# Performance work log

Hardware: AMD Instinct MI355X
Metric: run time of the kernel (lower is better)

Reference implementation:

```python
import jax, jax.numpy as jnp
import numpy as np

N = 100000
E = 3200000
IN_DIM = 512
HID = 256
NUM_CLASSES = 16
P_DROP = 0.5
EPS_BN = 1e-5


def setup_inputs() -> dict:
    key = jax.random.key(0)
    ks = jax.random.split(key, 6)
    x = jax.random.normal(ks[0], (N, IN_DIM), jnp.float32)
    edge_src = jax.random.randint(ks[1], (E,), 0, N, dtype=jnp.int32)
    edge_dst = jax.random.randint(ks[2], (E,), 0, N, dtype=jnp.int32)
    # Glorot-ish init for GraphConv weights (bias=False in the module)
    W1 = jax.random.normal(ks[3], (IN_DIM, HID), jnp.float32) / np.sqrt(IN_DIM).astype(np.float32)
    W2 = jax.random.normal(ks[4], (HID, NUM_CLASSES), jnp.float32) / np.sqrt(HID).astype(np.float32)
    W3 = jax.random.normal(ks[5], (HID, NUM_CLASSES), jnp.float32) / np.sqrt(HID).astype(np.float32)
    return {"x": x, "W1": W1, "W2": W2, "W3": W3,
            "edge_src": edge_src, "edge_dst": edge_dst}


def _graph_conv(h, W, edge_src, edge_dst, out_inv_sqrt, in_inv_sqrt):
    # DGL GraphConv, norm='both', bias=False:
    #   rst = D_in^{-1/2} * A_agg( D_out^{-1/2} * h @ W )
    # Apply W before aggregation (out_dim <= in_dim here); same math as DGL.
    h = h * out_inv_sqrt[:, None]          # [N, d_in]
    h = h @ W                              # [N, d_out]
    agg = jax.ops.segment_sum(h[edge_src], edge_dst, num_segments=h.shape[0])
    return agg * in_inv_sqrt[:, None]


def _dropout(key, x, p=P_DROP):
    keep = jax.random.bernoulli(key, 1.0 - p, x.shape)
    return jnp.where(keep, x / (1.0 - p), jnp.zeros((), x.dtype))


def reference(x, W1, W2, W3, edge_src, edge_dst):
    n = x.shape[0]
    ones = jnp.ones(edge_src.shape[0], x.dtype)
    out_deg = jax.ops.segment_sum(ones, edge_src, num_segments=n)
    in_deg = jax.ops.segment_sum(ones, edge_dst, num_segments=n)
    out_is = jnp.maximum(out_deg, 1.0) ** -0.5   # DGL clamps degree to min 1
    in_is = jnp.maximum(in_deg, 1.0) ** -0.5

    k1, k2a, k2b, keps = jax.random.split(jax.random.key(42), 4)

    # gc1 + relu
    h = _dropout(k1, x)
    h = jax.nn.relu(_graph_conv(h, W1, edge_src, edge_dst, out_is, in_is))

    # BatchNorm1d(affine=False, track_running_stats=False): batch stats
    mean = jnp.mean(h, axis=0)
    var = jnp.var(h, axis=0)
    h = (h - mean) * jax.lax.rsqrt(var + EPS_BN)

    # gc2 (mu) and gc3 (logvar), each with its own dropout of hidden1
    mu = _graph_conv(_dropout(k2a, h), W2, edge_src, edge_dst, out_is, in_is)
    logvar = _graph_conv(_dropout(k2b, h), W3, edge_src, edge_dst, out_is, in_is)

    # reparameterize (training): eps * exp(logvar) + mu  (note: exp(logvar), per source)
    eps = jax.random.normal(keps, mu.shape, mu.dtype)
    return eps * jnp.exp(logvar) + mu
```

## Files before the change

kernel.cpp:

```cpp
#include <hip/hip_runtime.h>
#include <stdint.h>

#define N_NODES 100000
#define N_EDGES 3200000
#define IN_DIM  512
#define HID     256
#define NCLS    16

#define DBLK   256
#define DCHUNK (N_EDGES / DBLK)
#define DWIN2  50000

typedef unsigned short u16;
typedef __attribute__((ext_vector_type(8))) short short8;
typedef __attribute__((ext_vector_type(4))) float float4v;

__device__ __forceinline__ float bf2f(u16 u) {
  return __uint_as_float(((uint32_t)u) << 16);
}
__device__ __forceinline__ u16 f2bf(float f) {
  uint32_t u = __float_as_uint(f);
  return (u16)((u + 0x7fffu + ((u >> 16) & 1u)) >> 16);
}
__device__ __forceinline__ void acc8(float* a, uint4 v) {
  a[0] += bf2f((u16)(v.x & 0xffffu)); a[1] += bf2f((u16)(v.x >> 16));
  a[2] += bf2f((u16)(v.y & 0xffffu)); a[3] += bf2f((u16)(v.y >> 16));
  a[4] += bf2f((u16)(v.z & 0xffffu)); a[5] += bf2f((u16)(v.z >> 16));
  a[6] += bf2f((u16)(v.w & 0xffffu)); a[7] += bf2f((u16)(v.w >> 16));
}

__device__ __forceinline__ void gload16(const void* g, void* l) {
  __builtin_amdgcn_global_load_lds(
      (const __attribute__((address_space(1))) uint32_t*)g,
      (__attribute__((address_space(3))) uint32_t*)l, 16, 0, 0);
}

__host__ __device__ __forceinline__ uint32_t rotl32(uint32_t v, int d) {
  return (v << d) | (v >> (32 - d));
}

__host__ __device__ __forceinline__ void threefry2x32(uint32_t k0, uint32_t k1,
    uint32_t x0, uint32_t x1, uint32_t& o0, uint32_t& o1) {
  uint32_t ks0 = k0, ks1 = k1, ks2 = k0 ^ k1 ^ 0x1BD11BDAu;
  x0 += ks0; x1 += ks1;
#define TF_R(r) { x0 += x1; x1 = rotl32(x1, r); x1 ^= x0; }
  TF_R(13) TF_R(15) TF_R(26) TF_R(6)
  x0 += ks1; x1 += ks2 + 1u;
  TF_R(17) TF_R(29) TF_R(16) TF_R(24)
  x0 += ks2; x1 += ks0 + 2u;
  TF_R(13) TF_R(15) TF_R(26) TF_R(6)
  x0 += ks0; x1 += ks1 + 3u;
  TF_R(17) TF_R(29) TF_R(16) TF_R(24)
  x0 += ks1; x1 += ks2 + 4u;
  TF_R(13) TF_R(15) TF_R(26) TF_R(6)
  x0 += ks2; x1 += ks0 + 5u;
#undef TF_R
  o0 = x0; o1 = x1;
}

__host__ __device__ __forceinline__ uint32_t tf_bits32(uint32_t k0, uint32_t k1, uint32_t idx) {
  uint32_t o0, o1;
  threefry2x32(k0, k1, 0u, idx, o0, o1);
  return o0 ^ o1;
}

__device__ __forceinline__ float erfinv_f32(float x) {
  float w = -log1pf(-x * x);
  float p;
  if (w < 5.0f) {
    w -= 2.5f;
    p = 2.81022636e-08f;
    p = fmaf(p, w, 3.43273939e-07f);
    p = fmaf(p, w, -3.5233877e-06f);
    p = fmaf(p, w, -4.39150654e-06f);
    p = fmaf(p, w, 0.00021858087f);
    p = fmaf(p, w, -0.00125372503f);
    p = fmaf(p, w, -0.00417768164f);
    p = fmaf(p, w, 0.246640727f);
    p = fmaf(p, w, 1.50140941f);
  } else {
    w = sqrtf(w) - 3.0f;
    p = -0.000200214257f;
    p = fmaf(p, w, 0.000100950558f);
    p = fmaf(p, w, 0.00134934322f);
    p = fmaf(p, w, -0.00367342844f);
    p = fmaf(p, w, 0.00573950773f);
    p = fmaf(p, w, -0.0076224613f);
    p = fmaf(p, w, 0.00943887047f);
    p = fmaf(p, w, 1.00167406f);
    p = fmaf(p, w, 2.83297682f);
  }
  return p * x;
}

__global__ __launch_bounds__(1024) void hist_k(
    const int* __restrict__ esrc, const int* __restrict__ edst,
    u16* __restrict__ P16) {
  __shared__ uint32_t h32[DWIN2 / 2];
  const int b = blockIdx.x, tid = threadIdx.x;
  const int ebase = b * DCHUNK;
  for (int w = 0; w < 2; ++w) {
    const int lo = w * DWIN2;
    for (int i = tid; i < DWIN2 / 2; i += 1024) h32[i] = 0u;
    __syncthreads();
    for (int e = ebase + tid; e < ebase + DCHUNK; e += 1024) {
      int s = esrc[e], d = edst[e];
      unsigned su = (unsigned)(s - lo);
      if (su < (unsigned)DWIN2) atomicAdd(&h32[su >> 1], 1u << ((su & 1) * 16));
      unsigned du = (unsigned)(d - lo);
      if (du < (unsigned)DWIN2) atomicAdd(&h32[du >> 1], 0x100u << ((du & 1) * 16));
    }
    __syncthreads();
    for (int i = tid; i < DWIN2 / 2; i += 1024) {
      *(uint32_t*)(P16 + (size_t)b * N_NODES + lo + 2 * i) = h32[i];
    }
    __syncthreads();
  }
}

__global__ void degsum_k(u16* __restrict__ P16, int* __restrict__ ind,
                         float* __restrict__ out_is, float* __restrict__ in_is) {
  int n = blockIdx.x * 256 + threadIdx.x;
  if (n >= N_NODES) return;
  uint32_t to = 0, ti = 0;
#pragma unroll 8
  for (int b = 0; b < DBLK; ++b) {
    uint32_t v = P16[(size_t)b * N_NODES + n];
    P16[(size_t)b * N_NODES + n] = (u16)ti;
    to += v & 0xffu; ti += v >> 8;
  }
  ind[n] = (int)ti;
  out_is[n] = rsqrtf(fmaxf((float)to, 1.0f));
  in_is[n]  = rsqrtf(fmaxf((float)ti, 1.0f));
}

__global__ __launch_bounds__(1024) void scan_offsets_k(
    const int* __restrict__ ind, int* __restrict__ row_ofs) {
  __shared__ int wsum[16];
  const int tid = threadIdx.x;
  const int lane = tid & 63, wv = tid >> 6;
  int running = 0;
  for (int base = 0; base < N_NODES; base += 1024) {
    const int i = base + tid;
    int v = (i < N_NODES) ? ind[i] : 0;
    int sc = v;
#pragma unroll
    for (int d = 1; d < 64; d <<= 1) {
      int t = __shfl_up(sc, d, 64);
      if (lane >= d) sc += t;
    }
    if (lane == 63) wsum[wv] = sc;
    __syncthreads();
    if (wv == 0) {
      int t = (lane < 16) ? wsum[lane] : 0;
#pragma unroll
      for (int d = 1; d < 16; d <<= 1) {
        int u = __shfl_up(t, d, 64);
        if (lane >= d) t += u;
      }
      if (lane < 16) wsum[lane] = t;
    }
    __syncthreads();
    int wbase = (wv > 0) ? wsum[wv - 1] : 0;
    if (i < N_NODES) row_ofs[i] = running + wbase + sc - v;
    running += wsum[15];
    __syncthreads();
  }
  if (tid == 0) row_ofs[N_NODES] = running;
}

__global__ __launch_bounds__(1024) void place_k(
    const int* __restrict__ esrc, const int* __restrict__ edst,
    const u16* __restrict__ P16, const int* __restrict__ row_ofs,
    int* __restrict__ csr) {
  __shared__ uint32_t cur32[N_NODES / 4];
  const int b = blockIdx.x, tid = threadIdx.x;
  for (int i = tid; i < N_NODES / 4; i += 1024) cur32[i] = 0u;
  __syncthreads();
  const int ebase = b * DCHUNK;
  for (int e = ebase + tid; e < ebase + DCHUNK; e += 1024) {
    int d = edst[e];
    int base = row_ofs[d] + (int)P16[(size_t)b * N_NODES + d];
    uint32_t old = atomicAdd(&cur32[d >> 2], 1u << ((d & 3) * 8));
    int c = (int)((old >> ((d & 3) * 8)) & 0xffu);
    csr[base + c] = esrc[e];
  }
}

__global__ void cast_w_k(const float* __restrict__ W1, const float* __restrict__ W2,
                         const float* __restrict__ W3, u16* __restrict__ W1t,
                         u16* __restrict__ Wt23) {
  int idx = blockIdx.x * blockDim.x + threadIdx.x;
  if (idx < IN_DIM * HID) {
    int k = idx >> 8, n = idx & 255;
    W1t[n * IN_DIM + k] = f2bf(W1[idx]);
  } else {
    int t = idx - IN_DIM * HID;
    int n = t >> 8, k = t & 255;
    float v = (n < 16) ? W2[k * NCLS + n] : W3[k * NCLS + (n - 16)];
    Wt23[n * HID + k] = f2bf(v);
  }
}

#define G1_BM 128
#define G1_BKC 8
__global__ __launch_bounds__(512, 2) void gemm1_k(
    const float* __restrict__ x, const float* __restrict__ out_is,
    uint32_t k0, uint32_t k1,
    const u16* __restrict__ W1t, u16* __restrict__ X1b) {
  __shared__ u16 As[G1_BM * 64];
  __shared__ u16 Bs[256 * 64];
  const int tid = threadIdx.x;
  const int wid = tid >> 6, lane = tid & 63;
  const int wr = wid >> 2, wc = wid & 3;
  const int m16 = lane & 15, q = lane >> 4;
  const int srow = lane >> 3, schunk = lane & 7;
  const long base_row = (long)blockIdx.x * G1_BM;

  const int arow_l = tid >> 2, acp = tid & 3;
  const long agrow = base_row + arow_l;
  const long asrow = (agrow < N_NODES) ? agrow : (N_NODES - 1);
  const float asc = 2.0f * out_is[asrow];
  const float* xrow = x + asrow * IN_DIM;
  const int aw0 = ((2 * acp)     ^ (arow_l & 7)) * 8;
  const int aw1 = ((2 * acp + 1) ^ (arow_l & 7)) * 8;

  float4v acc[4][4];
#pragma unroll
  for (int i = 0; i < 4; ++i)
#pragma unroll
    for (int j = 0; j < 4; ++j) acc[i][j] = (float4v)0.0f;

  for (int ks = 0; ks < IN_DIM / 64; ++ks) {
    const int kbase = ks * 64 + acp * 16;
    float4 f0 = *(const float4*)(xrow + kbase);
    float4 f1 = *(const float4*)(xrow + kbase + 4);
    float4 f2 = *(const float4*)(xrow + kbase + 8);
    float4 f3 = *(const float4*)(xrow + kbase + 12);
    float xv[16] = {f0.x, f0.y, f0.z, f0.w, f1.x, f1.y, f1.z, f1.w,
                    f2.x, f2.y, f2.z, f2.w, f3.x, f3.y, f3.z, f3.w};
    const uint32_t ibase = (uint32_t)asrow * IN_DIM + (uint32_t)kbase;
    u16 ob[16];
#pragma unroll
    for (int j = 0; j < 16; ++j) {
      uint32_t bits = tf_bits32(k0, k1, ibase + (uint32_t)j);
      ob[j] = f2bf((bits >> 31) ? 0.0f : xv[j] * asc);
    }
    uint4 pka, pkb;
    pka.x = (uint32_t)ob[0] | ((uint32_t)ob[1] << 16);
    pka.y = (uint32_t)ob[2] | ((uint32_t)ob[3] << 16);
    pka.z = (uint32_t)ob[4] | ((uint32_t)ob[5] << 16);
    pka.w = (uint32_t)ob[6] | ((uint32_t)ob[7] << 16);
    pkb.x = (uint32_t)ob[8] | ((uint32_t)ob[9] << 16);
    pkb.y = (uint32_t)ob[10] | ((uint32_t)ob[11] << 16);
    pkb.z = (uint32_t)ob[12] | ((uint32_t)ob[13] << 16);
    pkb.w = (uint32_t)ob[14] | ((uint32_t)ob[15] << 16);
    *(uint4*)(As + arow_l * 64 + aw0) = pka;
    *(uint4*)(As + arow_l * 64 + aw1) = pkb;
#pragma unroll
    for (int i = 0; i < 4; ++i) {
      int j = wid * 4 + i;
      int n = j * 8 + srow;
      int gch = ks * G1_BKC + (schunk ^ (n & 7));
      gload16(W1t + (size_t)n * IN_DIM + gch * 8, Bs + j * 512);
    }
    __syncthreads();
#pragma unroll
    for (int kk = 0; kk < 2; ++kk) {
      short8 a[4], b[4];
      const int kq = kk * 4 + q;
      const int c = kq ^ (m16 & 7);
#pragma unroll
      for (int rt = 0; rt < 4; ++rt) {
        int row = wr * 64 + rt * 16 + m16;
        a[rt] = *(const short8*)(As + row * 64 + c * 8);
      }
#pragma unroll
      for (int ct = 0; ct < 4; ++ct) {
        int n = wc * 64 + ct * 16 + m16;
        b[ct] = *(const short8*)(Bs + n * 64 + c * 8);
      }
#pragma unroll
      for (int rt = 0; rt < 4; ++rt)
#pragma unroll
        for (int ct = 0; ct < 4; ++ct)
          acc[rt][ct] = __builtin_amdgcn_mfma_f32_16x16x32_bf16(a[rt], b[ct], acc[rt][ct], 0, 0, 0);
    }
    __syncthreads();
  }
#pragma unroll
  for (int rt = 0; rt < 4; ++rt) {
#pragma unroll
    for (int r = 0; r < 4; ++r) {
      long grow = base_row + wr * 64 + rt * 16 + q * 4 + r;
      if (grow < N_NODES) {
#pragma unroll
        for (int ct = 0; ct < 4; ++ct)
          X1b[grow * HID + wc * 64 + ct * 16 + m16] = f2bf(acc[rt][ct][r]);
      }
    }
  }
}

__global__ __launch_bounds__(256) void agg_relu_k(
    const u16* __restrict__ X1b, const int* __restrict__ row_ofs,
    const int* __restrict__ csr, const float* __restrict__ in_is,
    u16* __restrict__ h1b) {
  int d = blockIdx.x * 4 + (threadIdx.x >> 6);
  int lane = threadIdx.x & 63;
  int half = lane >> 5;
  int col = (lane & 31) * 8;
  int beg = row_ofs[d], end = row_ofs[d + 1];
  float a[8];
#pragma unroll
  for (int i = 0; i < 8; ++i) a[i] = 0.0f;
  int j = beg + half;
  for (; j + 14 < end; j += 16) {
    int s0 = csr[j],      s1 = csr[j + 2],  s2 = csr[j + 4],  s3 = csr[j + 6];
    int s4 = csr[j + 8],  s5 = csr[j + 10], s6 = csr[j + 12], s7 = csr[j + 14];
    uint4 v0 = *(const uint4*)(X1b + (size_t)s0 * HID + col);
    uint4 v1 = *(const uint4*)(X1b + (size_t)s1 * HID + col);
    uint4 v2 = *(const uint4*)(X1b + (size_t)s2 * HID + col);
    uint4 v3 = *(const uint4*)(X1b + (size_t)s3 * HID + col);
    uint4 v4 = *(const uint4*)(X1b + (size_t)s4 * HID + col);
    uint4 v5 = *(const uint4*)(X1b + (size_t)s5 * HID + col);
    uint4 v6 = *(const uint4*)(X1b + (size_t)s6 * HID + col);
    uint4 v7 = *(const uint4*)(X1b + (size_t)s7 * HID + col);
    acc8(a, v0); acc8(a, v1); acc8(a, v2); acc8(a, v3);
    acc8(a, v4); acc8(a, v5); acc8(a, v6); acc8(a, v7);
  }
  for (; j + 6 < end; j += 8) {
    int s0 = csr[j], s1 = csr[j + 2], s2 = csr[j + 4], s3 = csr[j + 6];
    uint4 v0 = *(const uint4*)(X1b + (size_t)s0 * HID + col);
    uint4 v1 = *(const uint4*)(X1b + (size_t)s1 * HID + col);
    uint4 v2 = *(const uint4*)(X1b + (size_t)s2 * HID + col);
    uint4 v3 = *(const uint4*)(X1b + (size_t)s3 * HID + col);
    acc8(a, v0); acc8(a, v1); acc8(a, v2); acc8(a, v3);
  }
  for (; j < end; j += 2) {
    uint4 v0 = *(const uint4*)(X1b + (size_t)csr[j] * HID + col);
    acc8(a, v0);
  }
#pragma unroll
  for (int i = 0; i < 8; ++i) a[i] += __shfl(a[i], lane ^ 32, 64);
  if (half == 0) {
    float is = in_is[d];
    u16 o[8];
#pragma unroll
    for (int i = 0; i < 8; ++i) o[i] = f2bf(fmaxf(a[i] * is, 0.0f));
    uint4 pk;
    pk.x = (uint32_t)o[0] | ((uint32_t)o[1] << 16);
    pk.y = (uint32_t)o[2] | ((uint32_t)o[3] << 16);
    pk.z = (uint32_t)o[4] | ((uint32_t)o[5] << 16);
    pk.w = (uint32_t)o[6] | ((uint32_t)o[7] << 16);
    *(uint4*)(h1b + (size_t)d * HID + col) = pk;
  }
}

__global__ __launch_bounds__(256) void bn_stats_k(const u16* __restrict__ h1b,
                                                  float* __restrict__ bn) {
  __shared__ float ls[512];
  const int tid = threadIdx.x;
  const int cb = (tid & 31) * 8;
  const int ms = tid >> 5;
  float s[8], s2[8];
#pragma unroll
  for (int i = 0; i < 8; ++i) { s[i] = 0.f; s2[i] = 0.f; }
  for (int m = ms;; m += 8) {
    int r = blockIdx.x + 256 * m;
    if (r >= N_NODES) break;
    uint4 v = *(const uint4*)(h1b + (size_t)r * HID + cb);
    float f[8];
    f[0] = bf2f((u16)(v.x & 0xffffu)); f[1] = bf2f((u16)(v.x >> 16));
    f[2] = bf2f((u16)(v.y & 0xffffu)); f[3] = bf2f((u16)(v.y >> 16));
    f[4] = bf2f((u16)(v.z & 0xffffu)); f[5] = bf2f((u16)(v.z >> 16));
    f[6] = bf2f((u16)(v.w & 0xffffu)); f[7] = bf2f((u16)(v.w >> 16));
#pragma unroll
    for (int i = 0; i < 8; ++i) { s[i] += f[i]; s2[i] += f[i] * f[i]; }
  }
  ls[tid] = 0.f; ls[tid + 256] = 0.f;
  __syncthreads();
#pragma unroll
  for (int i = 0; i < 8; ++i) {
    atomicAdd(&ls[cb + i], s[i]);
    atomicAdd(&ls[256 + cb + i], s2[i]);
  }
  __syncthreads();
  atomicAdd(&bn[tid], ls[tid]);
  atomicAdd(&bn[HID + tid], ls[256 + tid]);
}

#define WLS 264
__global__ __launch_bounds__(256) void gemm23_k(
    const u16* __restrict__ h1b, const u16* __restrict__ Wt23,
    uint32_t ka0, uint32_t ka1, uint32_t kb0, uint32_t kb1,
    const float* __restrict__ out_is, const float* __restrict__ bn,
    u16* __restrict__ XMLV) {
  __shared__ u16 Wls[32 * WLS];
  __shared__ float cB[HID], cA[HID];
  const int tid = threadIdx.x;
#pragma unroll
  for (int i = 0; i < 4; ++i) {
    int idx = tid + i * 256;
    int n = idx >> 5, c = idx & 31;
    *(uint4*)(Wls + n * WLS + c * 8) = ((const uint4*)Wt23)[idx];
  }
  {
    float mean = bn[tid] * (1.0f / (float)N_NODES);
    float var = bn[HID + tid] * (1.0f / (float)N_NODES) - mean * mean;
    float istd = rsqrtf(var + 1e-5f);
    cB[tid] = istd;
    cA[tid] = -mean * istd;
  }
  __syncthreads();

  const int wv = tid >> 6, lane = tid & 63;
  const int m = lane & 15, q = lane >> 4;
  const long arow = (long)blockIdx.x * 64 + wv * 16 + m;
  const bool valid = arow < N_NODES;
  const float osc = valid ? 2.0f * out_is[arow] : 0.0f;
  const uint32_t rbase = (uint32_t)(valid ? arow : 0) * HID;

  float4v accM = (float4v)0.0f, accL = (float4v)0.0f;
  for (int kc = 0; kc < HID; kc += 32) {
    const int kof = kc + q * 8;
    uint4 hv = make_uint4(0, 0, 0, 0);
    if (valid) hv = *(const uint4*)(h1b + arow * HID + kof);
    float4 B0 = *(const float4*)(cB + kof);
    float4 B1 = *(const float4*)(cB + kof + 4);
    float4 A0 = *(const float4*)(cA + kof);
    float4 A1 = *(const float4*)(cA + kof + 4);
    float hval[8] = {
      bf2f((u16)(hv.x & 0xffffu)), bf2f((u16)(hv.x >> 16)),
      bf2f((u16)(hv.y & 0xffffu)), bf2f((u16)(hv.y >> 16)),
      bf2f((u16)(hv.z & 0xffffu)), bf2f((u16)(hv.z >> 16)),
      bf2f((u16)(hv.w & 0xffffu)), bf2f((u16)(hv.w >> 16))};
    float nb[8] = {B0.x, B0.y, B0.z, B0.w, B1.x, B1.y, B1.z, B1.w};
    float na[8] = {A0.x, A0.y, A0.z, A0.w, A1.x, A1.y, A1.z, A1.w};
    const uint32_t ibase = rbase + (uint32_t)kof;
    short8 Aa, Ab;
#pragma unroll
    for (int jj = 0; jj < 8; ++jj) {
      float t = fmaf(hval[jj], nb[jj], na[jj]) * osc;
      u16 tb = f2bf(t);
      uint32_t ba = tf_bits32(ka0, ka1, ibase + (uint32_t)jj);
      uint32_t bb = tf_bits32(kb0, kb1, ibase + (uint32_t)jj);
      Aa[jj] = (short)((ba >> 31) ? 0 : tb);
      Ab[jj] = (short)((bb >> 31) ? 0 : tb);
    }
    short8 Bm = *(const short8*)(Wls + m * WLS + kof);
    short8 Bl = *(const short8*)(Wls + (16 + m) * WLS + kof);
    accM = __builtin_amdgcn_mfma_f32_16x16x32_bf16(Aa, Bm, accM, 0, 0, 0);
    accL = __builtin_amdgcn_mfma_f32_16x16x32_bf16(Ab, Bl, accL, 0, 0, 0);
  }
#pragma unroll
  for (int r = 0; r < 4; ++r) {
    long srow = (long)blockIdx.x * 64 + wv * 16 + q * 4 + r;
    if (srow < N_NODES) {
      XMLV[srow * 32 + m]      = f2bf(accM[r]);
      XMLV[srow * 32 + 16 + m] = f2bf(accL[r]);
    }
  }
}

__global__ __launch_bounds__(256) void agg_final_k(
    const u16* __restrict__ XMLV, const int* __restrict__ row_ofs,
    const int* __restrict__ csr, const float* __restrict__ in_is,
    uint32_t ke0, uint32_t ke1, float* __restrict__ out) {
  int g = blockIdx.x * 4 + (threadIdx.x >> 6);
  int lane = threadIdx.x & 63;
  int half = lane >> 5, c = lane & 31;
  int beg = row_ofs[g], end = row_ofs[g + 1];
  float s = 0.f;
  int j = beg + half;
  for (; j + 14 < end; j += 16) {
    int s0 = csr[j],      s1 = csr[j + 2],  s2 = csr[j + 4],  s3 = csr[j + 6];
    int s4 = csr[j + 8],  s5 = csr[j + 10], s6 = csr[j + 12], s7 = csr[j + 14];
    float v0 = bf2f(XMLV[(size_t)s0 * 32 + c]);
    float v1 = bf2f(XMLV[(size_t)s1 * 32 + c]);
    float v2 = bf2f(XMLV[(size_t)s2 * 32 + c]);
    float v3 = bf2f(XMLV[(size_t)s3 * 32 + c]);
    float v4 = bf2f(XMLV[(size_t)s4 * 32 + c]);
    float v5 = bf2f(XMLV[(size_t)s5 * 32 + c]);
    float v6 = bf2f(XMLV[(size_t)s6 * 32 + c]);
    float v7 = bf2f(XMLV[(size_t)s7 * 32 + c]);
    s += v0; s += v1; s += v2; s += v3;
    s += v4; s += v5; s += v6; s += v7;
  }
#pragma unroll
  for (int k = 0; k < 8; ++k) {
    int e = j + 2 * k;
    if (e < end) s += bf2f(XMLV[(size_t)csr[e] * 32 + c]);
  }
  s += __shfl(s, lane ^ 32, 64);
  if (half == 0) {
    s *= in_is[g];
    float other = __shfl(s, lane ^ 16, 64);
    if (c < 16) {
      uint32_t i = (uint32_t)(g * NCLS + c);
      uint32_t bits = tf_bits32(ke0, ke1, i);
      float f = __uint_as_float((bits >> 9) | 0x3f800000u) - 1.0f;
      const float lo = -0.99999994f;
      float u = fmaxf(lo, fmaf(f, 2.0f, lo));
      float eps = 1.41421356f * erfinv_f32(u);
      out[i] = eps * expf(other) + s;
    }
  }
}

extern "C" void kernel_launch(void* const* d_in, const int* in_sizes, int n_in,
                              void* d_out, int out_size, void* d_ws, size_t ws_size,
                              hipStream_t stream) {
  (void)in_sizes; (void)n_in; (void)out_size; (void)ws_size;
  const float* x  = (const float*)d_in[0];
  const float* W1 = (const float*)d_in[1];
  const float* W2 = (const float*)d_in[2];
  const float* W3 = (const float*)d_in[3];
  const int* esrc = (const int*)d_in[4];
  const int* edst = (const int*)d_in[5];
  float* out = (float*)d_out;

  uint32_t kb[8];
  for (int j = 0; j < 4; ++j)
    threefry2x32(0u, 42u, 0u, (uint32_t)j, kb[2 * j], kb[2 * j + 1]);

  char* p = (char*)d_ws;
  auto take = [&](size_t bytes) -> void* {
    void* r = (void*)p;
    p += (bytes + 255) & ~(size_t)255;
    return r;
  };
  u16* P16       = (u16*)take(sizeof(u16) * (size_t)DBLK * N_NODES);
  u16* X1b       = (u16*)take(sizeof(u16) * (size_t)N_NODES * HID);
  u16* h1b       = (u16*)take(sizeof(u16) * (size_t)N_NODES * HID);
  u16* XMLV      = (u16*)take(sizeof(u16) * (size_t)N_NODES * 32);
  u16* W1t       = (u16*)take(sizeof(u16) * (size_t)IN_DIM * HID);
  u16* Wt23      = (u16*)take(sizeof(u16) * 32 * HID);
  int* in_deg    = (int*)take(sizeof(int) * N_NODES);
  float* out_is  = (float*)take(sizeof(float) * N_NODES);
  float* in_is   = (float*)take(sizeof(float) * N_NODES);
  int* row_ofs   = (int*)take(sizeof(int) * (N_NODES + 1));
  int* csr       = (int*)take(sizeof(int) * N_EDGES);
  float* bn      = (float*)take(sizeof(float) * 1024);

  hipMemsetAsync(bn, 0, sizeof(float) * 512, stream);

  hist_k<<<DBLK, 1024, 0, stream>>>(esrc, edst, P16);
  degsum_k<<<(N_NODES + 255) / 256, 256, 0, stream>>>(P16, in_deg, out_is, in_is);
  scan_offsets_k<<<1, 1024, 0, stream>>>(in_deg, row_ofs);
  place_k<<<DBLK, 1024, 0, stream>>>(esrc, edst, P16, row_ofs, csr);

  cast_w_k<<<(IN_DIM * HID + 32 * HID) / 256, 256, 0, stream>>>(W1, W2, W3, W1t, Wt23);

  gemm1_k<<<(N_NODES + G1_BM - 1) / G1_BM, 512, 0, stream>>>(x, out_is, kb[0], kb[1], W1t, X1b);
  agg_relu_k<<<N_NODES / 4, 256, 0, stream>>>(X1b, row_ofs, csr, in_is, h1b);
  bn_stats_k<<<256, 256, 0, stream>>>(h1b, bn);
  gemm23_k<<<(N_NODES + 63) / 64, 256, 0, stream>>>(h1b, Wt23, kb[2], kb[3], kb[4], kb[5],
                                                    out_is, bn, XMLV);
  agg_final_k<<<N_NODES / 4, 256, 0, stream>>>(XMLV, row_ofs, csr, in_is, kb[6], kb[7], out);
}
```

Before: 1.019 ms.

## Build CSR via bucketed two-pass partition and parallel multi-block prefix scan

```diff
diff --git a/kernel.cpp b/kernel.cpp
--- a/kernel.cpp
+++ b/kernel.cpp
@@ -10,6 +10,8 @@
 #define DBLK   256
 #define DCHUNK (N_EDGES / DBLK)
 #define DWIN2  50000
+#define NBKT   98
+#define NTILE  ((N_NODES + 255) / 256)
 
 typedef unsigned short u16;
 typedef __attribute__((ext_vector_type(8))) short short8;
@@ -95,10 +97,12 @@
 
 __global__ __launch_bounds__(1024) void hist_k(
     const int* __restrict__ esrc, const int* __restrict__ edst,
-    u16* __restrict__ P16) {
+    u16* __restrict__ P16, uint32_t* __restrict__ bofs_g) {
   __shared__ uint32_t h32[DWIN2 / 2];
+  __shared__ uint32_t bcnt[NBKT + 1];
   const int b = blockIdx.x, tid = threadIdx.x;
   const int ebase = b * DCHUNK;
+  if (tid < NBKT + 1) bcnt[tid] = 0u;
   for (int w = 0; w < 2; ++w) {
     const int lo = w * DWIN2;
     for (int i = tid; i < DWIN2 / 2; i += 1024) h32[i] = 0u;
@@ -109,6 +113,7 @@
       if (su < (unsigned)DWIN2) atomicAdd(&h32[su >> 1], 1u << ((su & 1) * 16));
       unsigned du = (unsigned)(d - lo);
       if (du < (unsigned)DWIN2) atomicAdd(&h32[du >> 1], 0x100u << ((du & 1) * 16));
+      if (w == 0) atomicAdd(&bcnt[d >> 10], 1u);
     }
     __syncthreads();
     for (int i = tid; i < DWIN2 / 2; i += 1024) {
@@ -116,74 +121,99 @@
     }
     __syncthreads();
   }
-}
-
-__global__ void degsum_k(u16* __restrict__ P16, int* __restrict__ ind,
-                         float* __restrict__ out_is, float* __restrict__ in_is) {
-  int n = blockIdx.x * 256 + threadIdx.x;
-  if (n >= N_NODES) return;
+  if (tid == 0) {
+    uint32_t run = 0;
+    for (int k = 0; k < NBKT; ++k) { uint32_t c = bcnt[k]; bcnt[k] = run; run += c; }
+    bcnt[NBKT] = run;
+  }
+  __syncthreads();
+  if (tid < NBKT + 1) bofs_g[b * (NBKT + 1) + tid] = bcnt[tid];
+}
+
+__global__ void degsum_k(const u16* __restrict__ P16, float* __restrict__ out_is,
+                         float* __restrict__ in_is, int* __restrict__ row_ofs,
+                         int* __restrict__ tile_sum) {
+  const int tid = threadIdx.x;
+  const int n = blockIdx.x * 256 + tid;
+  const int lane = tid & 63, wv = tid >> 6;
   uint32_t to = 0, ti = 0;
+  if (n < N_NODES) {
 #pragma unroll 8
-  for (int b = 0; b < DBLK; ++b) {
-    uint32_t v = P16[(size_t)b * N_NODES + n];
-    P16[(size_t)b * N_NODES + n] = (u16)ti;
-    to += v & 0xffu; ti += v >> 8;
-  }
-  ind[n] = (int)ti;
-  out_is[n] = rsqrtf(fmaxf((float)to, 1.0f));
-  in_is[n]  = rsqrtf(fmaxf((float)ti, 1.0f));
-}
-
-__global__ __launch_bounds__(1024) void scan_offsets_k(
-    const int* __restrict__ ind, int* __restrict__ row_ofs) {
-  __shared__ int wsum[16];
-  const int tid = threadIdx.x;
+    for (int b = 0; b < DBLK; ++b) {
+      uint32_t v = P16[(size_t)b * N_NODES + n];
+      to += v & 0xffu; ti += v >> 8;
+    }
+    out_is[n] = rsqrtf(fmaxf((float)to, 1.0f));
+    in_is[n]  = rsqrtf(fmaxf((float)ti, 1.0f));
+  }
+  int sc = (int)ti;
+#pragma unroll
+  for (int d = 1; d < 64; d <<= 1) {
+    int t = __shfl_up(sc, d, 64);
+    if (lane >= d) sc += t;
+  }
+  __shared__ int ws[4];
+  if (lane == 63) ws[wv] = sc;
+  __syncthreads();
+  int wbase = 0;
+#pragma unroll
+  for (int i = 0; i < 4; ++i) if (i < wv) wbase += ws[i];
+  if (n < N_NODES) row_ofs[n] = wbase + sc - (int)ti;
+  if (tid == 0) tile_sum[blockIdx.x] = ws[0] + ws[1] + ws[2] + ws[3];
+}
+
+__global__ void fixup_k(const int* __restrict__ tile_sum, int* __restrict__ row_ofs) {
+  const int b = blockIdx.x, tid = threadIdx.x;
   const int lane = tid & 63, wv = tid >> 6;
-  int running = 0;
-  for (int base = 0; base < N_NODES; base += 1024) {
-    const int i = base + tid;
-    int v = (i < N_NODES) ? ind[i] : 0;
-    int sc = v;
-#pragma unroll
-    for (int d = 1; d < 64; d <<= 1) {
-      int t = __shfl_up(sc, d, 64);
-      if (lane >= d) sc += t;
-    }
-    if (lane == 63) wsum[wv] = sc;
-    __syncthreads();
-    if (wv == 0) {
-      int t = (lane < 16) ? wsum[lane] : 0;
-#pragma unroll
-      for (int d = 1; d < 16; d <<= 1) {
-        int u = __shfl_up(t, d, 64);
-        if (lane >= d) t += u;
-      }
-      if (lane < 16) wsum[lane] = t;
-    }
-    __syncthreads();
-    int wbase = (wv > 0) ? wsum[wv - 1] : 0;
-    if (i < N_NODES) row_ofs[i] = running + wbase + sc - v;
-    running += wsum[15];
-    __syncthreads();
-  }
-  if (tid == 0) row_ofs[N_NODES] = running;
-}
-
-__global__ __launch_bounds__(1024) void place_k(
+  int v = 0;
+  if (tid < b) v = tile_sum[tid];
+  if (tid + 256 < b) v += tile_sum[tid + 256];
+#pragma unroll
+  for (int m = 1; m < 64; m <<= 1) v += __shfl_xor(v, m, 64);
+  __shared__ int wr[4];
+  if (lane == 0) wr[wv] = v;
+  __syncthreads();
+  const int base = wr[0] + wr[1] + wr[2] + wr[3];
+  const int n = b * 256 + tid;
+  if (n < N_NODES) row_ofs[n] += base;
+  if (b == (int)gridDim.x - 1 && tid == 0) row_ofs[N_NODES] = base + tile_sum[b];
+}
+
+__global__ __launch_bounds__(1024) void partition_k(
     const int* __restrict__ esrc, const int* __restrict__ edst,
-    const u16* __restrict__ P16, const int* __restrict__ row_ofs,
-    int* __restrict__ csr) {
-  __shared__ uint32_t cur32[N_NODES / 4];
+    const uint32_t* __restrict__ bofs_g, unsigned long long* __restrict__ ebuf) {
+  __shared__ uint32_t bcur[NBKT];
   const int b = blockIdx.x, tid = threadIdx.x;
-  for (int i = tid; i < N_NODES / 4; i += 1024) cur32[i] = 0u;
+  if (tid < NBKT) bcur[tid] = bofs_g[b * (NBKT + 1) + tid];
   __syncthreads();
   const int ebase = b * DCHUNK;
   for (int e = ebase + tid; e < ebase + DCHUNK; e += 1024) {
-    int d = edst[e];
-    int base = row_ofs[d] + (int)P16[(size_t)b * N_NODES + d];
-    uint32_t old = atomicAdd(&cur32[d >> 2], 1u << ((d & 3) * 8));
-    int c = (int)((old >> ((d & 3) * 8)) & 0xffu);
-    csr[base + c] = esrc[e];
+    int d = edst[e], s = esrc[e];
+    uint32_t slot = atomicAdd(&bcur[d >> 10], 1u);
+    ebuf[(size_t)b * DCHUNK + slot] = ((unsigned long long)(uint32_t)s << 32) | (uint32_t)d;
+  }
+}
+
+__global__ __launch_bounds__(1024) void bplace_k(
+    const unsigned long long* __restrict__ ebuf, const uint32_t* __restrict__ bofs_g,
+    const int* __restrict__ row_ofs, int* __restrict__ csr) {
+  __shared__ uint32_t cur[1024];
+  const int k = blockIdx.x, tid = threadIdx.x;
+  const int lane = tid & 63, wv = tid >> 6;
+  const int dbase = k << 10;
+  int nd = N_NODES - dbase; if (nd > 1024) nd = 1024;
+  if (tid < nd) cur[tid] = (uint32_t)row_ofs[dbase + tid];
+  __syncthreads();
+  for (int b = wv; b < DBLK; b += 16) {
+    uint32_t st = bofs_g[b * (NBKT + 1) + k];
+    uint32_t en = bofs_g[b * (NBKT + 1) + k + 1];
+    for (uint32_t i = st + lane; i < en; i += 64) {
+      unsigned long long v = ebuf[(size_t)b * DCHUNK + i];
+      int d = (int)(uint32_t)(v & 0xffffffffu);
+      int s = (int)(uint32_t)(v >> 32);
+      uint32_t slot = atomicAdd(&cur[d - dbase], 1u);
+      csr[slot] = s;
+    }
   }
 }
 
@@ -531,12 +561,14 @@
     return r;
   };
   u16* P16       = (u16*)take(sizeof(u16) * (size_t)DBLK * N_NODES);
+  unsigned long long* ebuf = (unsigned long long*)take(sizeof(unsigned long long) * (size_t)N_EDGES);
   u16* X1b       = (u16*)take(sizeof(u16) * (size_t)N_NODES * HID);
   u16* h1b       = (u16*)take(sizeof(u16) * (size_t)N_NODES * HID);
   u16* XMLV      = (u16*)take(sizeof(u16) * (size_t)N_NODES * 32);
   u16* W1t       = (u16*)take(sizeof(u16) * (size_t)IN_DIM * HID);
   u16* Wt23      = (u16*)take(sizeof(u16) * 32 * HID);
-  int* in_deg    = (int*)take(sizeof(int) * N_NODES);
+  uint32_t* bofs_g = (uint32_t*)take(sizeof(uint32_t) * (size_t)DBLK * (NBKT + 1));
+  int* tile_sum  = (int*)take(sizeof(int) * NTILE);
   float* out_is  = (float*)take(sizeof(float) * N_NODES);
   float* in_is   = (float*)take(sizeof(float) * N_NODES);
   int* row_ofs   = (int*)take(sizeof(int) * (N_NODES + 1));
@@ -545,10 +577,11 @@
 
   hipMemsetAsync(bn, 0, sizeof(float) * 512, stream);
 
-  hist_k<<<DBLK, 1024, 0, stream>>>(esrc, edst, P16);
-  degsum_k<<<(N_NODES + 255) / 256, 256, 0, stream>>>(P16, in_deg, out_is, in_is);
-  scan_offsets_k<<<1, 1024, 0, stream>>>(in_deg, row_ofs);
-  place_k<<<DBLK, 1024, 0, stream>>>(esrc, edst, P16, row_ofs, csr);
+  hist_k<<<DBLK, 1024, 0, stream>>>(esrc, edst, P16, bofs_g);
+  degsum_k<<<NTILE, 256, 0, stream>>>(P16, out_is, in_is, row_ofs, tile_sum);
+  fixup_k<<<NTILE, 256, 0, stream>>>(tile_sum, row_ofs);
+  partition_k<<<DBLK, 1024, 0, stream>>>(esrc, edst, bofs_g, ebuf);
+  bplace_k<<<NBKT, 1024, 0, stream>>>(ebuf, bofs_g, row_ofs, csr);
 
   cast_w_k<<<(IN_DIM * HID + 32 * HID) / 256, 256, 0, stream>>>(W1, W2, W3, W1t, Wt23);
 
```

Result: faster. 912.8 us (-10.4%).
